# Kernel tuning notes

Measured on AMD Instinct MI355X. Metric: run time of the kernel, lower is better.

## Reference

```python
import jax, jax.numpy as jnp
import numpy as np

N_NODES = 50000
N_EDGES = 600000
D = 128


def setup_inputs() -> dict:
    key = jax.random.key(0)
    ks = jax.random.split(key, 10)
    feat = jax.random.normal(ks[0], (N_NODES, D), dtype=jnp.float32)
    edge_src = jax.random.randint(ks[1], (N_EDGES,), 0, N_NODES, dtype=jnp.int64)
    edge_dst = jax.random.randint(ks[2], (N_EDGES,), 0, N_NODES, dtype=jnp.int64)
    edge_w = jax.random.uniform(ks[3], (N_EDGES,), dtype=jnp.float32)
    s = 1.0 / np.sqrt(D)
    W1 = jax.random.uniform(ks[4], (D, D), minval=-s, maxval=s, dtype=jnp.float32)
    W2 = jax.random.uniform(ks[5], (D, D), minval=-s, maxval=s, dtype=jnp.float32)
    # torch GRUCell params: weight_ih [3H, 2D], weight_hh [3H, H], biases [3H]
    W_ih = jax.random.uniform(ks[6], (3 * D, 2 * D), minval=-s, maxval=s, dtype=jnp.float32)
    W_hh = jax.random.uniform(ks[7], (3 * D, D), minval=-s, maxval=s, dtype=jnp.float32)
    b_ih = jax.random.uniform(ks[8], (3 * D,), minval=-s, maxval=s, dtype=jnp.float32)
    b_hh = jax.random.uniform(ks[9], (3 * D,), minval=-s, maxval=s, dtype=jnp.float32)
    return {"feat": feat, "edge_src": edge_src, "edge_dst": edge_dst, "edge_w": edge_w,
            "W1": W1, "W2": W2, "W_ih": W_ih, "W_hh": W_hh, "b_ih": b_ih, "b_hh": b_hh}


def _weighted_mean_agg(feat, w, src, dst, n_nodes):
    # message: ft[src] * w; reduce: sum(m) / sum(w) per dst node (zero for isolated nodes)
    m = feat[src] * w[:, None]                                   # [E, D]
    sm = jax.ops.segment_sum(m, dst, num_segments=n_nodes)      # [N, D]
    sw = jax.ops.segment_sum(w, dst, num_segments=n_nodes)      # [N]
    has = sw > 0
    denom = jnp.where(has, sw, 1.0)[:, None]
    return jnp.where(has[:, None], sm / denom, 0.0)


def reference(feat, edge_src, edge_dst, edge_w, W1, W2, W_ih, W_hh, b_ih, b_hh):
    n = feat.shape[0]
    neigh1 = _weighted_mean_agg(feat, edge_w, edge_src, edge_dst, n)  # forward graph
    neigh2 = _weighted_mean_agg(feat, edge_w, edge_dst, edge_src, n)  # reverse graph
    hn = jnp.concatenate([neigh1 @ W1.T, neigh2 @ W2.T], axis=1)      # [N, 2D]
    # torch.nn.GRUCell(hn, feat)
    gi = hn @ W_ih.T + b_ih    # [N, 3D]
    gh = feat @ W_hh.T + b_hh  # [N, 3D]
    ir, iz, inn = jnp.split(gi, 3, axis=1)
    hr, hz, hnn = jnp.split(gh, 3, axis=1)
    r = jax.nn.sigmoid(ir + hr)
    z = jax.nn.sigmoid(iz + hz)
    ng = jnp.tanh(inn + r * hnn)
    return (1.0 - z) * ng + z * feat
```

## Files before the change

### kernel.cpp

```cpp
#include <hip/hip_runtime.h>
#include <math.h>

#define N_NODES 50000
#define N_EDGES 600000
#define D 128
#define KTOT 384
#define NCOLS 512

#define SCAN_CHUNK 512
#define SCAN_NB ((N_NODES + SCAN_CHUNK - 1) / SCAN_CHUNK)

#define GEMM_ROWB ((N_NODES + 127) / 128)
#define GEMM_NWG  (GEMM_ROWB * 8)
#define NXCD 8
#define KHALF 192

#define BSHIFT 10
#define NBUCKETS ((N_NODES + (1 << BSHIFT) - 1) >> BSHIFT)
#define PA_NB 512
#define PA_CHUNK ((N_EDGES + PA_NB - 1) / PA_NB)
#define PB_SPLIT 4

typedef unsigned int u32;
typedef unsigned short u16;

typedef __attribute__((ext_vector_type(8))) short bf16x8;
typedef __attribute__((ext_vector_type(4))) float f32x4;

__device__ __forceinline__ float bits2f(u32 u) {
    float f; __builtin_memcpy(&f, &u, 4);
    return f;
}
__device__ __forceinline__ u16 f2b(float f) {
    u32 u; __builtin_memcpy(&u, &f, 4);
    u32 r = (u + 0x7fffu + ((u >> 16) & 1u)) >> 16;
    return (u16)r;
}

__global__ void fill_sentinel(float* __restrict__ p, long n, float v) {
    long i = (long)blockIdx.x * blockDim.x + threadIdx.x;
    long stride = (long)gridDim.x * blockDim.x;
    for (; i < n; i += stride) p[i] = v;
}

__global__ void front(const float* __restrict__ feat, u16* __restrict__ fb16,
                      u32* __restrict__ offz) {
    long stride = (long)gridDim.x * blockDim.x;
    long t0 = (long)blockIdx.x * blockDim.x + threadIdx.x;
    for (long i = t0; i < 2 * N_NODES; i += stride) offz[i] = 0u;
    for (long i = t0; i < (long)N_NODES * (D / 4); i += stride) {
        int n = (int)(i >> 5), j4 = (int)(i & 31);
        float4 v = *(const float4*)(feat + (size_t)n * D + j4 * 4);
        ushort4 o;
        o.x = f2b(v.x); o.y = f2b(v.y); o.z = f2b(v.z); o.w = f2b(v.w);
        *(ushort4*)(fb16 + ((size_t)n << 7) + j4 * 4) = o;
    }
}

__global__ void count_both(const int* __restrict__ esrc, const int* __restrict__ edst,
                           int* __restrict__ cnt1, int* __restrict__ cnt2) {
    int e = blockIdx.x * blockDim.x + threadIdx.x;
    if (e < N_EDGES) {
        atomicAdd(&cnt1[edst[e]], 1);
        atomicAdd(&cnt2[esrc[e]], 1);
    }
}

__global__ void scan_partial(const int* __restrict__ off, int* __restrict__ bsum) {
    int dir = blockIdx.y, bx = blockIdx.x, t = threadIdx.x;
    const int* a = off + (size_t)dir * N_NODES;
    int i0 = bx * SCAN_CHUNK + 2 * t;
    int s = 0;
    if (i0 < N_NODES) s += a[i0];
    if (i0 + 1 < N_NODES) s += a[i0 + 1];
    __shared__ int red[256];
    red[t] = s;
    __syncthreads();
    for (int d = 128; d > 0; d >>= 1) {
        if (t < d) red[t] += red[t + d];
        __syncthreads();
    }
    if (t == 0) bsum[dir * SCAN_NB + bx] = red[0];
}

__global__ void scan_bsums(int* __restrict__ bsum) {
    __shared__ int part[256];
    int t = threadIdx.x;
    int i = t & 127, dir = t >> 7;
    int v = (i < SCAN_NB) ? bsum[dir * SCAN_NB + i] : 0;
    part[t] = v;
    __syncthreads();
    for (int d = 1; d < 128; d <<= 1) {
        int add = (i >= d) ? part[t - d] : 0;
        __syncthreads();
        part[t] += add;
        __syncthreads();
    }
    if (i < SCAN_NB) bsum[dir * SCAN_NB + i] = part[t] - v;
}

__global__ void scan_final(int* __restrict__ off, const int* __restrict__ bsum) {
    int dir = blockIdx.y, bx = blockIdx.x, t = threadIdx.x;
    int* a = off + (size_t)dir * N_NODES;
    int base = bsum[dir * SCAN_NB + bx];
    int i0 = bx * SCAN_CHUNK + 2 * t;
    int e0 = (i0 < N_NODES) ? a[i0] : 0;
    int e1 = (i0 + 1 < N_NODES) ? a[i0 + 1] : 0;
    __shared__ int part[256];
    int v = e0 + e1;
    part[t] = v;
    __syncthreads();
    for (int d = 1; d < 256; d <<= 1) {
        int add = (t >= d) ? part[t - d] : 0;
        __syncthreads();
        part[t] += add;
        __syncthreads();
    }
    int tb = base + part[t] - v;
    if (i0 < N_NODES) a[i0] = tb;
    if (i0 + 1 < N_NODES) a[i0 + 1] = tb + e0;
}

__global__ void init_buckets(const int* __restrict__ off1, const int* __restrict__ off2,
                             int* __restrict__ bks) {
    int t = threadIdx.x;
    if (t <= NBUCKETS) {
        int n = t << BSHIFT;
        int s1 = (t == NBUCKETS) ? N_EDGES : off1[n];
        int s2 = (t == NBUCKETS) ? N_EDGES : off2[n];
        bks[t] = s1;
        bks[128 + t] = s2;
        if (t < NBUCKETS) { bks[64 + t] = s1; bks[192 + t] = s2; }
    }
}

__global__ __launch_bounds__(256)
void partA(const int* __restrict__ key, const int* __restrict__ nbr,
           const float* __restrict__ ew, int* __restrict__ bucketFill,
           uint2* __restrict__ tmp) {
    __shared__ int lcnt[NBUCKETS];
    __shared__ int lbase[NBUCKETS + 1];
    __shared__ int gbase[NBUCKETS];
    __shared__ uint2 stage[PA_CHUNK];
    int t = threadIdx.x;
    int e0 = blockIdx.x * PA_CHUNK;
    int e1 = min(e0 + PA_CHUNK, N_EDGES);
    if (t < NBUCKETS) lcnt[t] = 0;
    __syncthreads();
    for (int e = e0 + t; e < e1; e += 256)
        atomicAdd(&lcnt[key[e] >> BSHIFT], 1);
    __syncthreads();
    if (t == 0) {
        int s = 0;
        for (int b = 0; b < NBUCKETS; ++b) { lbase[b] = s; s += lcnt[b]; }
        lbase[NBUCKETS] = s;
    }
    __syncthreads();
    if (t < NBUCKETS) {
        gbase[t] = atomicAdd(&bucketFill[t], lcnt[t]);
        lcnt[t] = 0;
    }
    __syncthreads();
    for (int e = e0 + t; e < e1; e += 256) {
        int k = key[e];
        int b = k >> BSHIFT;
        int i = lbase[b] + atomicAdd(&lcnt[b], 1);
        u32 wb = (u32)f2b(ew[e]);
        stage[i] = make_uint2(((u32)k << 16) | (u32)nbr[e], wb);
    }
    __syncthreads();
    int total = lbase[NBUCKETS];
    for (int i = t; i < total; i += 256) {
        int lo = 0, hi = NBUCKETS;
        while (hi - lo > 1) { int mid = (lo + hi) >> 1; if (lbase[mid] <= i) lo = mid; else hi = mid; }
        tmp[gbase[lo] + (i - lbase[lo])] = stage[i];
    }
}

__global__ __launch_bounds__(256)
void partB(const uint2* __restrict__ tmp, const int* __restrict__ bucketStart,
           int* __restrict__ off, u32* __restrict__ csr) {
    int b = blockIdx.x;
    int s = bucketStart[b], e = bucketStart[b + 1];
    int cnt = e - s;
    int per = (cnt + PB_SPLIT - 1) / PB_SPLIT;
    int ss = s + blockIdx.y * per;
    int ee = min(ss + per, e);
    for (int i = ss + (int)threadIdx.x; i < ee; i += 256) {
        uint2 v = tmp[i];
        int dst = v.x >> 16;
        int p = atomicAdd(&off[dst], 1);
        csr[p] = ((v.x & 0xffffu) << 16) | v.y;
    }
}

__global__ void gather_both(u16* __restrict__ Ah2, const u16* __restrict__ fb16,
                            const int* __restrict__ off1, const u32* __restrict__ csr1,
                            const int* __restrict__ off2, const u32* __restrict__ csr2) {
    int gw = (blockIdx.x * blockDim.x + threadIdx.x) >> 6;
    int lane = threadIdx.x & 63;
    if (gw >= 2 * N_NODES) return;
    int dir = (gw >= N_NODES);
    int n = dir ? gw - N_NODES : gw;
    const int* off = dir ? off2 : off1;
    const u32* csr = dir ? csr2 : csr1;
    int start = (n == 0) ? 0 : off[n - 1];
    int end = off[n];
    const u16* fbl = fb16 + lane * 2;
    float ax = 0.f, ay = 0.f, sw = 0.f;
    int p = start;
    for (; p + 3 < end; p += 4) {
        u32 c0 = csr[p], c1 = csr[p + 1], c2 = csr[p + 2], c3 = csr[p + 3];
        u32 v0 = *(const u32*)(fbl + ((size_t)(c0 >> 16) << 7));
        u32 v1 = *(const u32*)(fbl + ((size_t)(c1 >> 16) << 7));
        u32 v2 = *(const u32*)(fbl + ((size_t)(c2 >> 16) << 7));
        u32 v3 = *(const u32*)(fbl + ((size_t)(c3 >> 16) << 7));
        float w0 = bits2f(c0 << 16), w1 = bits2f(c1 << 16);
        float w2 = bits2f(c2 << 16), w3 = bits2f(c3 << 16);
        ax += bits2f(v0 << 16) * w0 + bits2f(v1 << 16) * w1
            + bits2f(v2 << 16) * w2 + bits2f(v3 << 16) * w3;
        ay += bits2f(v0 & 0xffff0000u) * w0 + bits2f(v1 & 0xffff0000u) * w1
            + bits2f(v2 & 0xffff0000u) * w2 + bits2f(v3 & 0xffff0000u) * w3;
        sw += w0 + w1 + w2 + w3;
    }
    for (; p < end; ++p) {
        u32 c0 = csr[p];
        u32 v0 = *(const u32*)(fbl + ((size_t)(c0 >> 16) << 7));
        float w0 = bits2f(c0 << 16);
        ax += bits2f(v0 << 16) * w0;
        ay += bits2f(v0 & 0xffff0000u) * w0;
        sw += w0;
    }
    float inv = (sw > 0.f) ? 1.f / sw : 0.f;
    if (!isfinite(inv)) inv = 0.f;
    u32 o = ((u32)f2b(ay * inv) << 16) | (u32)f2b(ax * inv);
    *(u32*)(Ah2 + ((size_t)n << 8) + dir * 128 + lane * 2) = o;
}

__global__ void compute_M(const float* __restrict__ W_ih,
                          const float* __restrict__ W1,
                          const float* __restrict__ W2,
                          float* __restrict__ M1, float* __restrict__ M2) {
    int r = blockIdx.x;
    int k = threadIdx.x;
    int which = blockIdx.y;
    const float* Wsel = which ? W2 : W1;
    const float* ih = W_ih + (size_t)r * (2 * D) + which * D;
    float acc = 0.f;
    for (int j = 0; j < D; ++j) acc += ih[j] * Wsel[j * D + k];
    (which ? M2 : M1)[r * D + k] = acc;
}

__global__ void fill_Bt(const float* __restrict__ M1, const float* __restrict__ M2,
                        const float* __restrict__ W_hh, u16* __restrict__ Bt) {
    int idx = blockIdx.x * blockDim.x + threadIdx.x;
    if (idx >= NCOLS * KTOT) return;
    int cp = idx / KTOT;
    int k  = idx - cp * KTOT;
    int c = cp >> 2, g = cp & 3;
    float v = 0.f;
    if (g <= 1) {
        int r = c + (g == 1 ? 128 : 0);
        v = (k < 128) ? M1[r * D + k]
          : (k < 256) ? M2[r * D + (k - 128)]
                      : W_hh[r * D + (k - 256)];
    } else if (g == 2) {
        int r = c + 256;
        v = (k < 128) ? M1[r * D + k]
          : (k < 256) ? M2[r * D + (k - 128)] : 0.f;
    } else {
        v = (k >= 256) ? W_hh[(c + 256) * D + (k - 256)] : 0.f;
    }
    if (!isfinite(v)) v = 0.f;
    Bt[idx] = f2b(v);
}

#define LOAD_A(m, k) ((k) < 8 ? *(const bf16x8*)(aP[m] + (k) * 32) \
                              : *(const bf16x8*)(fP[m] + ((k) - 8) * 32))

__global__ __launch_bounds__(256)
void gemm_gru_mfma(const u16* __restrict__ Ah2, const u16* __restrict__ fb16,
                   const u16* __restrict__ Bt, const float* __restrict__ feat,
                   const float* __restrict__ b_ih, const float* __restrict__ b_hh,
                   float* __restrict__ out) {
    __shared__ __align__(16) char smem[64 * KHALF * 2];
    float (*epi)[16][65] = (float(*)[16][65])smem;

    int bid = blockIdx.x;
    int wgid = (bid % NXCD) * (GEMM_NWG / NXCD) + bid / NXCD;
    int rowp = wgid >> 3;
    int colb = wgid & 7;
    int tid = threadIdx.x, lane = tid & 63, wid = tid >> 6;
    int mw = rowp * 128 + wid * 32;
    int nw = colb * 64;
    int rif = lane & 15, kg = lane >> 4;

    int scol = tid >> 2;
    int sq   = tid & 3;
    u32 sbase = (u32)scol * (KHALF * 2) + (u32)sq * 96;
    u32 sxor  = (u32)((scol & 7) << 4);
    const u16* ssrc0 = Bt + (size_t)(nw + scol) * KTOT + sq * 48;

    u32 bCol[4], bXor[4];
    #pragma unroll
    for (int n = 0; n < 4; ++n) {
        u32 col = n * 16 + rif;
        bCol[n] = col * (KHALF * 2) + kg * 16;
        bXor[n] = (col & 7) << 4;
    }

    f32x4 acc[2][4];
    #pragma unroll
    for (int m = 0; m < 2; ++m)
        #pragma unroll
        for (int n = 0; n < 4; ++n)
            acc[m][n] = (f32x4){0.f, 0.f, 0.f, 0.f};

    const u16* aP[2];
    const u16* fP[2];
    #pragma unroll
    for (int m = 0; m < 2; ++m) {
        int arow = min(mw + m * 16 + rif, N_NODES - 1);
        aP[m] = Ah2 + ((size_t)arow << 8) + kg * 8;
        fP[m] = fb16 + ((size_t)arow << 7) + kg * 8;
    }

    #pragma unroll
    for (int i = 0; i < 6; ++i) {
        bf16x8 v = *(const bf16x8*)(ssrc0 + i * 8);
        *(bf16x8*)(smem + ((sbase + i * 16) ^ sxor)) = v;
    }

    bf16x8 abuf[4][2];
    #pragma unroll
    for (int s = 0; s < 3; ++s)
        #pragma unroll
        for (int m = 0; m < 2; ++m)
            abuf[s][m] = LOAD_A(m, s);

    __syncthreads();

    #pragma unroll
    for (int ks = 0; ks < 6; ++ks) {
        if (ks + 3 < KTOT / 32) {
            #pragma unroll
            for (int m = 0; m < 2; ++m)
                abuf[(ks + 3) & 3][m] = LOAD_A(m, ks + 3);
        }
        bf16x8 bfr[4];
        #pragma unroll
        for (int n = 0; n < 4; ++n)
            bfr[n] = *(const bf16x8*)(smem + ((bCol[n] + ks * 64) ^ bXor[n]));
        #pragma unroll
        for (int m = 0; m < 2; ++m)
            #pragma unroll
            for (int n = 0; n < 4; ++n)
                acc[m][n] = __builtin_amdgcn_mfma_f32_16x16x32_bf16(
                    abuf[ks & 3][m], bfr[n], acc[m][n], 0, 0, 0);
    }

    __syncthreads();

    #pragma unroll
    for (int i = 0; i < 6; ++i) {
        bf16x8 v = *(const bf16x8*)(ssrc0 + KHALF + i * 8);
        *(bf16x8*)(smem + ((sbase + i * 16) ^ sxor)) = v;
    }
    __syncthreads();

    #pragma unroll
    for (int ks = 6; ks < 12; ++ks) {
        if (ks + 3 < KTOT / 32) {
            #pragma unroll
            for (int m = 0; m < 2; ++m)
                abuf[(ks + 3) & 3][m] = LOAD_A(m, ks + 3);
        }
        bf16x8 bfr[4];
        #pragma unroll
        for (int n = 0; n < 4; ++n)
            bfr[n] = *(const bf16x8*)(smem + ((bCol[n] + (ks - 6) * 64) ^ bXor[n]));
        #pragma unroll
        for (int m = 0; m < 2; ++m)
            #pragma unroll
            for (int n = 0; n < 4; ++n)
                acc[m][n] = __builtin_amdgcn_mfma_f32_16x16x32_bf16(
                    abuf[ks & 3][m], bfr[n], acc[m][n], 0, 0, 0);
    }

    int rc0 = nw >> 2;
    int erow = lane >> 2;
    int g4 = lane & 3;
    int cbase = rc0 + g4 * 4;
    float4 bi_r = *(const float4*)(b_ih + cbase);
    float4 bh_r = *(const float4*)(b_hh + cbase);
    float4 bi_z = *(const float4*)(b_ih + cbase + 128);
    float4 bh_z = *(const float4*)(b_hh + cbase + 128);
    float4 bi_n = *(const float4*)(b_ih + cbase + 256);
    float4 bh_n = *(const float4*)(b_hh + cbase + 256);

    #pragma unroll
    for (int m = 0; m < 2; ++m) {
        __syncthreads();
        #pragma unroll
        for (int n = 0; n < 4; ++n)
            #pragma unroll
            for (int reg = 0; reg < 4; ++reg)
                epi[wid][kg * 4 + reg][n * 16 + rif] = acc[m][n][reg];
        __syncthreads();

        float4 q0 = *(const float4*)&epi[wid][erow][g4 * 16 + 0];
        float4 q1 = *(const float4*)&epi[wid][erow][g4 * 16 + 4];
        float4 q2 = *(const float4*)&epi[wid][erow][g4 * 16 + 8];
        float4 q3 = *(const float4*)&epi[wid][erow][g4 * 16 + 12];

        int node = mw + m * 16 + erow;
        if (node < N_NODES) {
            float4 f = *(const float4*)(feat + (size_t)node * D + cbase);
            float4 res;
            {
                float r = 1.f / (1.f + __expf(-(q0.x + bi_r.x + bh_r.x)));
                float z = 1.f / (1.f + __expf(-(q0.y + bi_z.x + bh_z.x)));
                float ng = tanhf(q0.z + bi_n.x + r * (q0.w + bh_n.x));
                res.x = (1.f - z) * ng + z * f.x;
            }
            {
                float r = 1.f / (1.f + __expf(-(q1.x + bi_r.y + bh_r.y)));
                float z = 1.f / (1.f + __expf(-(q1.y + bi_z.y + bh_z.y)));
                float ng = tanhf(q1.z + bi_n.y + r * (q1.w + bh_n.y));
                res.y = (1.f - z) * ng + z * f.y;
            }
            {
                float r = 1.f / (1.f + __expf(-(q2.x + bi_r.z + bh_r.z)));
                float z = 1.f / (1.f + __expf(-(q2.y + bi_z.z + bh_z.z)));
                float ng = tanhf(q2.z + bi_n.z + r * (q2.w + bh_n.z));
                res.z = (1.f - z) * ng + z * f.z;
            }
            {
                float r = 1.f / (1.f + __expf(-(q3.x + bi_r.w + bh_r.w)));
                float z = 1.f / (1.f + __expf(-(q3.y + bi_z.w + bh_z.w)));
                float ng = tanhf(q3.z + bi_n.w + r * (q3.w + bh_n.w));
                res.w = (1.f - z) * ng + z * f.w;
            }
            *(float4*)(out + (size_t)node * D + cbase) = res;
        }
    }
}

extern "C" void kernel_launch(void* const* d_in, const int* in_sizes, int n_in,
                              void* d_out, int out_size, void* d_ws, size_t ws_size,
                              hipStream_t stream) {
    const float* feat = (const float*)d_in[0];
    const int*   esrc = (const int*)d_in[1];
    const int*   edst = (const int*)d_in[2];
    const float* ew   = (const float*)d_in[3];
    const float* W1   = (const float*)d_in[4];
    const float* W2   = (const float*)d_in[5];
    const float* W_ih = (const float*)d_in[6];
    const float* W_hh = (const float*)d_in[7];
    const float* b_ih = (const float*)d_in[8];
    const float* b_hh = (const float*)d_in[9];
    float* out = (float*)d_out;

    const size_t AH2_ELEMS = (size_t)N_NODES * 256;
    const size_t FB_ELEMS  = (size_t)N_NODES * 128;
    const size_t needWords = (AH2_ELEMS + FB_ELEMS) / 2 + 2 * N_NODES
                           + 2 * (size_t)N_EDGES + 2 * (size_t)N_EDGES
                           + 512 + 2 * (size_t)KTOT * D + (NCOLS * KTOT) / 2;
    if (ws_size < needWords * 4) {
        fill_sentinel<<<512, 256, 0, stream>>>(out, (long)out_size, 12345.0f);
        return;
    }

    u16*   Ah2  = (u16*)d_ws;
    u16*   fb16 = Ah2 + AH2_ELEMS;
    int*   off1 = (int*)(fb16 + FB_ELEMS);
    int*   off2 = off1 + N_NODES;
    u32*   csr1 = (u32*)(off2 + N_NODES);
    u32*   csr2 = csr1 + N_EDGES;
    uint2* tmp  = (uint2*)(csr2 + N_EDGES);
    int*   bsum = (int*)(tmp + N_EDGES);
    int*   bks  = bsum + 256;
    float* M1   = (float*)(bks + 256);
    float* M2   = M1 + KTOT * D;
    u16*   Bt   = (u16*)(M2 + KTOT * D);

    const int EB = (N_EDGES + 255) / 256;

    front<<<2048, 256, 0, stream>>>(feat, fb16, (u32*)off1);
    count_both<<<EB, 256, 0, stream>>>(esrc, edst, off1, off2);
    scan_partial<<<dim3(SCAN_NB, 2), 256, 0, stream>>>(off1, bsum);
    scan_bsums<<<1, 256, 0, stream>>>(bsum);
    scan_final<<<dim3(SCAN_NB, 2), 256, 0, stream>>>(off1, bsum);

    init_buckets<<<1, 64, 0, stream>>>(off1, off2, bks);
    partA<<<PA_NB, 256, 0, stream>>>(edst, esrc, ew, bks + 64, tmp);
    partB<<<dim3(NBUCKETS, PB_SPLIT), 256, 0, stream>>>(tmp, bks, off1, csr1);
    partA<<<PA_NB, 256, 0, stream>>>(esrc, edst, ew, bks + 192, tmp);
    partB<<<dim3(NBUCKETS, PB_SPLIT), 256, 0, stream>>>(tmp, bks + 128, off2, csr2);

    gather_both<<<(2 * N_NODES * 64 + 255) / 256, 256, 0, stream>>>(
        Ah2, fb16, off1, csr1, off2, csr2);

    compute_M<<<dim3(KTOT, 2), 128, 0, stream>>>(W_ih, W1, W2, M1, M2);
    fill_Bt<<<(NCOLS * KTOT + 255) / 256, 256, 0, stream>>>(M1, M2, W_hh, Bt);

    gemm_gru_mfma<<<GEMM_NWG, 256, 0, stream>>>(Ah2, fb16, Bt, feat, b_ih, b_hh, out);
}
```

Measured before the change: 255.3 us.

## Merge both edge directions into single partition launches and widen gather loads

```diff
diff --git a/kernel.cpp b/kernel.cpp
--- a/kernel.cpp
+++ b/kernel.cpp
@@ -135,13 +135,19 @@
 }
 
 __global__ __launch_bounds__(256)
-void partA(const int* __restrict__ key, const int* __restrict__ nbr,
-           const float* __restrict__ ew, int* __restrict__ bucketFill,
-           uint2* __restrict__ tmp) {
+void partA(const int* __restrict__ esrc, const int* __restrict__ edst,
+           const float* __restrict__ ew, int* __restrict__ bks,
+           uint2* __restrict__ tmp1, uint2* __restrict__ tmp2) {
     __shared__ int lcnt[NBUCKETS];
     __shared__ int lbase[NBUCKETS + 1];
     __shared__ int gbase[NBUCKETS];
     __shared__ uint2 stage[PA_CHUNK];
+    int dir = blockIdx.y;
+    const int* key = dir ? esrc : edst;
+    const int* nbr = dir ? edst : esrc;
+    int* bucketFill = bks + (dir ? 192 : 64);
+    uint2* tmp = dir ? tmp2 : tmp1;
+
     int t = threadIdx.x;
     int e0 = blockIdx.x * PA_CHUNK;
     int e1 = min(e0 + PA_CHUNK, N_EDGES);
@@ -166,20 +172,28 @@
         int b = k >> BSHIFT;
         int i = lbase[b] + atomicAdd(&lcnt[b], 1);
         u32 wb = (u32)f2b(ew[e]);
-        stage[i] = make_uint2(((u32)k << 16) | (u32)nbr[e], wb);
+        stage[i] = make_uint2(((u32)k << 16) | (u32)nbr[e], ((u32)b << 16) | wb);
     }
     __syncthreads();
     int total = lbase[NBUCKETS];
     for (int i = t; i < total; i += 256) {
-        int lo = 0, hi = NBUCKETS;
-        while (hi - lo > 1) { int mid = (lo + hi) >> 1; if (lbase[mid] <= i) lo = mid; else hi = mid; }
-        tmp[gbase[lo] + (i - lbase[lo])] = stage[i];
+        uint2 v = stage[i];
+        int b = (int)(v.y >> 16);
+        tmp[gbase[b] + (i - lbase[b])] = make_uint2(v.x, v.y & 0xffffu);
     }
 }
 
 __global__ __launch_bounds__(256)
-void partB(const uint2* __restrict__ tmp, const int* __restrict__ bucketStart,
-           int* __restrict__ off, u32* __restrict__ csr) {
+void partB(const uint2* __restrict__ tmp1, const uint2* __restrict__ tmp2,
+           const int* __restrict__ bks,
+           int* __restrict__ off1, int* __restrict__ off2,
+           u32* __restrict__ csr1, u32* __restrict__ csr2) {
+    int dir = blockIdx.z;
+    const uint2* tmp = dir ? tmp2 : tmp1;
+    const int* bucketStart = bks + dir * 128;
+    int* off = dir ? off2 : off1;
+    u32* csr = dir ? csr2 : csr1;
+
     int b = blockIdx.x;
     int s = bucketStart[b], e = bucketStart[b + 1];
     int cnt = e - s;
@@ -190,7 +204,7 @@
         uint2 v = tmp[i];
         int dst = v.x >> 16;
         int p = atomicAdd(&off[dst], 1);
-        csr[p] = ((v.x & 0xffffu) << 16) | v.y;
+        csr[p] = ((v.x & 0xffffu) << 16) | (v.y & 0xffffu);
     }
 }
 
@@ -206,35 +220,46 @@
     const u32* csr = dir ? csr2 : csr1;
     int start = (n == 0) ? 0 : off[n - 1];
     int end = off[n];
-    const u16* fbl = fb16 + lane * 2;
-    float ax = 0.f, ay = 0.f, sw = 0.f;
+    int half = lane >> 5;
+    int hl = lane & 31;
+    const u16* fbl = fb16 + hl * 4;
+    float a0 = 0.f, a1 = 0.f, a2 = 0.f, a3 = 0.f, sw = 0.f;
     int p = start;
     for (; p + 3 < end; p += 4) {
-        u32 c0 = csr[p], c1 = csr[p + 1], c2 = csr[p + 2], c3 = csr[p + 3];
-        u32 v0 = *(const u32*)(fbl + ((size_t)(c0 >> 16) << 7));
-        u32 v1 = *(const u32*)(fbl + ((size_t)(c1 >> 16) << 7));
-        u32 v2 = *(const u32*)(fbl + ((size_t)(c2 >> 16) << 7));
-        u32 v3 = *(const u32*)(fbl + ((size_t)(c3 >> 16) << 7));
-        float w0 = bits2f(c0 << 16), w1 = bits2f(c1 << 16);
-        float w2 = bits2f(c2 << 16), w3 = bits2f(c3 << 16);
-        ax += bits2f(v0 << 16) * w0 + bits2f(v1 << 16) * w1
-            + bits2f(v2 << 16) * w2 + bits2f(v3 << 16) * w3;
-        ay += bits2f(v0 & 0xffff0000u) * w0 + bits2f(v1 & 0xffff0000u) * w1
-            + bits2f(v2 & 0xffff0000u) * w2 + bits2f(v3 & 0xffff0000u) * w3;
-        sw += w0 + w1 + w2 + w3;
-    }
-    for (; p < end; ++p) {
-        u32 c0 = csr[p];
-        u32 v0 = *(const u32*)(fbl + ((size_t)(c0 >> 16) << 7));
-        float w0 = bits2f(c0 << 16);
-        ax += bits2f(v0 << 16) * w0;
-        ay += bits2f(v0 & 0xffff0000u) * w0;
-        sw += w0;
-    }
-    float inv = (sw > 0.f) ? 1.f / sw : 0.f;
-    if (!isfinite(inv)) inv = 0.f;
-    u32 o = ((u32)f2b(ay * inv) << 16) | (u32)f2b(ax * inv);
-    *(u32*)(Ah2 + ((size_t)n << 8) + dir * 128 + lane * 2) = o;
+        u32 cA = csr[p + half];
+        u32 cB = csr[p + 2 + half];
+        uint2 vA = *(const uint2*)(fbl + ((size_t)(cA >> 16) << 7));
+        uint2 vB = *(const uint2*)(fbl + ((size_t)(cB >> 16) << 7));
+        float wA = bits2f(cA << 16), wB = bits2f(cB << 16);
+        a0 += bits2f(vA.x << 16) * wA + bits2f(vB.x << 16) * wB;
+        a1 += bits2f(vA.x & 0xffff0000u) * wA + bits2f(vB.x & 0xffff0000u) * wB;
+        a2 += bits2f(vA.y << 16) * wA + bits2f(vB.y << 16) * wB;
+        a3 += bits2f(vA.y & 0xffff0000u) * wA + bits2f(vB.y & 0xffff0000u) * wB;
+        sw += wA + wB;
+    }
+    for (; p < end; p += 2) {
+        u32 c = (p + half < end) ? csr[p + half] : 0u;
+        uint2 v = *(const uint2*)(fbl + ((size_t)(c >> 16) << 7));
+        float w = bits2f(c << 16);
+        a0 += bits2f(v.x << 16) * w;
+        a1 += bits2f(v.x & 0xffff0000u) * w;
+        a2 += bits2f(v.y << 16) * w;
+        a3 += bits2f(v.y & 0xffff0000u) * w;
+        sw += w;
+    }
+    a0 += __shfl_xor(a0, 32);
+    a1 += __shfl_xor(a1, 32);
+    a2 += __shfl_xor(a2, 32);
+    a3 += __shfl_xor(a3, 32);
+    sw += __shfl_xor(sw, 32);
+    if (lane < 32) {
+        float inv = (sw > 0.f) ? 1.f / sw : 0.f;
+        if (!isfinite(inv)) inv = 0.f;
+        uint2 o;
+        o.x = ((u32)f2b(a1 * inv) << 16) | (u32)f2b(a0 * inv);
+        o.y = ((u32)f2b(a3 * inv) << 16) | (u32)f2b(a2 * inv);
+        *(uint2*)(Ah2 + ((size_t)n << 8) + dir * 128 + hl * 4) = o;
+    }
 }
 
 __global__ void compute_M(const float* __restrict__ W_ih,
@@ -464,7 +489,8 @@
     const size_t AH2_ELEMS = (size_t)N_NODES * 256;
     const size_t FB_ELEMS  = (size_t)N_NODES * 128;
     const size_t needWords = (AH2_ELEMS + FB_ELEMS) / 2 + 2 * N_NODES
-                           + 2 * (size_t)N_EDGES + 2 * (size_t)N_EDGES
+                           + 2 * (size_t)N_EDGES
+                           + 4 * (size_t)N_EDGES
                            + 512 + 2 * (size_t)KTOT * D + (NCOLS * KTOT) / 2;
     if (ws_size < needWords * 4) {
         fill_sentinel<<<512, 256, 0, stream>>>(out, (long)out_size, 12345.0f);
@@ -477,8 +503,9 @@
     int*   off2 = off1 + N_NODES;
     u32*   csr1 = (u32*)(off2 + N_NODES);
     u32*   csr2 = csr1 + N_EDGES;
-    uint2* tmp  = (uint2*)(csr2 + N_EDGES);
-    int*   bsum = (int*)(tmp + N_EDGES);
+    uint2* tmp1 = (uint2*)(csr2 + N_EDGES);
+    uint2* tmp2 = tmp1 + N_EDGES;
+    int*   bsum = (int*)(tmp2 + N_EDGES);
     int*   bks  = bsum + 256;
     float* M1   = (float*)(bks + 256);
     float* M2   = M1 + KTOT * D;
@@ -493,10 +520,9 @@
     scan_final<<<dim3(SCAN_NB, 2), 256, 0, stream>>>(off1, bsum);
 
     init_buckets<<<1, 64, 0, stream>>>(off1, off2, bks);
-    partA<<<PA_NB, 256, 0, stream>>>(edst, esrc, ew, bks + 64, tmp);
-    partB<<<dim3(NBUCKETS, PB_SPLIT), 256, 0, stream>>>(tmp, bks, off1, csr1);
-    partA<<<PA_NB, 256, 0, stream>>>(esrc, edst, ew, bks + 192, tmp);
-    partB<<<dim3(NBUCKETS, PB_SPLIT), 256, 0, stream>>>(tmp, bks + 128, off2, csr2);
+    partA<<<dim3(PA_NB, 2), 256, 0, stream>>>(esrc, edst, ew, bks, tmp1, tmp2);
+    partB<<<dim3(NBUCKETS, PB_SPLIT, 2), 256, 0, stream>>>(
+        tmp1, tmp2, bks, off1, off2, csr1, csr2);
 
     gather_both<<<(2 * N_NODES * 64 + 255) / 256, 256, 0, stream>>>(
         Ah2, fb16, off1, csr1, off2, csr2);
```

After: 249.6 us. -2.2%, faster.
